# Kernel tuning notes

Measured on AMD Instinct MI355X. Metric: run time of the kernel, lower is better.

The kernel has to match this reference:

```python
import jax, jax.numpy as jnp
import numpy as np

A, B, K, P, STRIDE, ITERS = 32, 32, 3, 4, 2, 3
PSIZE = P * P
EPS = 1e-8


def add_patches(x):
    # x: (b, h, w, A*PSIZE) -> (b*oh*ow, K*K*A, PSIZE)
    b, h, w, c = x.shape
    oh = (h - K) // STRIDE + 1
    ow = (w - K) // STRIDE + 1
    idx = jnp.arange(oh) * STRIDE  # same for w since h == w here
    idx = idx[:, None] + jnp.arange(K)[None, :]          # (oh, K)
    p = x[:, idx]                                        # (b, oh, K, w, c)
    p = p[:, :, :, idx]                                  # (b, oh, K, ow, K, c)
    p = jnp.transpose(p, (0, 1, 3, 2, 4, 5))             # (b, oh, ow, K, K, c)
    p = p.reshape(b * oh * ow, K * K * A, PSIZE)
    return p, oh, ow


def transform_view(p_in, weights):
    # p_in: (N, K*K*A, PSIZE); weights: (K*K*A, B, P, P)
    N = p_in.shape[0]
    x = p_in.reshape(N, K * K * A, P, P)
    # pose matmul per (input capsule i, output type j): x[n,i] @ w[i,j]
    v = jnp.einsum('nipr,ijrq->nijpq', x, weights)       # (N, KKA, B, P, P)
    return v.reshape(N, K * K * A, B, PSIZE)


def squash(p):
    n2 = jnp.sum(p * p, axis=-1, keepdims=True)
    return p * n2 / (1.0 + n2) / jnp.sqrt(n2 + EPS)


def dynamic_routing(v, iters):
    # v: (N, KKA, B, PSIZE); inverted dynamic routing: softmax over input capsules
    N, KKA, Bt, _ = v.shape
    logits = jnp.zeros((N, KKA, Bt, 1), dtype=v.dtype)
    p = None
    for i in range(iters):
        r = jax.nn.softmax(logits, axis=1)               # route over input capsules
        p = squash(jnp.sum(r * v, axis=1, keepdims=True))  # (N,1,B,PSIZE)
        if i < iters - 1:
            logits = logits + jnp.sum(v * p, axis=-1, keepdims=True)
    return p[:, 0]                                       # (N, B, PSIZE)


def setup_inputs() -> dict:
    key = jax.random.key(0)
    k1, k2 = jax.random.split(key)
    x = jax.random.normal(k1, (2, 32, 32, A * PSIZE), dtype=jnp.float32)
    weights = jax.random.normal(k2, (K * K * A, B, P, P), dtype=jnp.float32)
    return {"x": x, "weights": weights}


def reference(x, weights):
    b = x.shape[0]
    p_in, oh, ow = add_patches(x)
    v = transform_view(p_in, weights)                    # (b*oh*ow, KKA, B, PSIZE)
    p_out = dynamic_routing(v, ITERS)                    # (b*oh*ow, B, PSIZE)
    return p_out.reshape(b, oh, ow, B * PSIZE)
```

## Files before the change

kernel.cpp:

```cpp
#include <hip/hip_runtime.h>


#define OH 15
#define OW 15
#define EPS_ 1e-8f

#define XT_ELEMS (2 * 32 * 32 * 512)
#define WT_ELEMS (32 * 5 * 64 * 16)

typedef float v2f __attribute__((ext_vector_type(2)));

__device__ __forceinline__ v2f pfma(float a, v2f b, v2f c) {
    return __builtin_elementwise_fma((v2f){a, a}, b, c);
}
__device__ __forceinline__ float b_lo(unsigned int u) {
    union { unsigned int i; float f; } c; c.i = u << 16; return c.f;
}
__device__ __forceinline__ float b_hi(unsigned int u) {
    union { unsigned int i; float f; } c; c.i = u & 0xFFFF0000u; return c.f;
}
__device__ __forceinline__ unsigned short f2bf(float f) {
    union { float f; unsigned int i; } c; c.f = f;
    return (unsigned short)((c.i + 0x7FFFu + ((c.i >> 16) & 1u)) >> 16);
}

__device__ __forceinline__ float dppx1(float x) {
    return __builtin_bit_cast(float, __builtin_amdgcn_update_dpp(
        0, __builtin_bit_cast(int, x), 0xB1, 0xF, 0xF, true));
}
__device__ __forceinline__ float dppx2(float x) {
    return __builtin_bit_cast(float, __builtin_amdgcn_update_dpp(
        0, __builtin_bit_cast(int, x), 0x4E, 0xF, 0xF, true));
}
template <int OFF>
__device__ __forceinline__ float swzx(float x) {
    return __builtin_bit_cast(float, __builtin_amdgcn_ds_swizzle(
        __builtin_bit_cast(int, x), OFF));
}
__device__ __forceinline__ float rdlane(float x, int q) {
    return __builtin_bit_cast(float, __builtin_amdgcn_readlane(
        __builtin_bit_cast(int, x), q));
}

__global__ __launch_bounds__(256) void stage_kernel(
    const float* __restrict__ x, const float* __restrict__ w,
    unsigned short* __restrict__ xt, unsigned short* __restrict__ wt)
{
    const int tid = blockIdx.x * 256 + threadIdx.x;
    if (tid < XT_ELEMS) {
        xt[tid] = f2bf(x[tid]);
    } else {
        const int t2 = tid - XT_ELEMS;
        const int j  = t2 / 5120;
        const int r  = t2 - j * 5120;
        const int k  = r >> 10;
        const int L  = (r >> 4) & 63;
        const int e  = r & 15;
        const int i  = L + 64 * k;
        wt[t2] = (i < 288) ? f2bf(w[(size_t)i * 512 + j * 16 + e])
                           : (unsigned short)0;
    }
}

template <bool PERM>
__global__ __launch_bounds__(64, 3) void convcaps_kernel(
    const void* __restrict__ xp,
    const void* __restrict__ wp_,
    float* __restrict__ out)
{
    const int blk  = blockIdx.x;
    const int n    = blk >> 5;
    const int j    = blk & 31;
    const int lane = threadIdx.x;

    const int batch = n / (OH * OW);
    const int rem   = n - batch * OH * OW;
    const int oy    = rem / OW;
    const int ox    = rem - oy * OW;

    const bool has5 = (lane < 32);

    v2f v[5][8];
    float logit[5] = {0.f, 0.f, 0.f, 0.f, has5 ? 0.f : -1e30f};

#pragma unroll
    for (int k = 0; k < 5; ++k) {
        if (k == 4 && !has5) {
#pragma unroll
            for (int m = 0; m < 8; ++m) v[4][m] = (v2f){0.f, 0.f};
        } else {
            const int i  = lane + 64 * k;
            const int a  = i & 31;
            const int kw = (i >> 5) % 3;
            const int kh = i / 96;
            const int h  = oy * 2 + kh;
            const int wc = ox * 2 + kw;
            const int pixel = (batch * 32 + h) * 32 + wc;

            float xr[16];
            v2f wr2[4][2];
            if (PERM) {
                const uint4* xb = reinterpret_cast<const uint4*>(
                    (const unsigned short*)xp + ((size_t)pixel * 512 + a * 16));
                uint4 u0 = xb[0], u1 = xb[1];
                xr[0]=b_lo(u0.x); xr[1]=b_hi(u0.x); xr[2]=b_lo(u0.y); xr[3]=b_hi(u0.y);
                xr[4]=b_lo(u0.z); xr[5]=b_hi(u0.z); xr[6]=b_lo(u0.w); xr[7]=b_hi(u0.w);
                xr[8]=b_lo(u1.x); xr[9]=b_hi(u1.x); xr[10]=b_lo(u1.y); xr[11]=b_hi(u1.y);
                xr[12]=b_lo(u1.z); xr[13]=b_hi(u1.z); xr[14]=b_lo(u1.w); xr[15]=b_hi(u1.w);
                const uint4* wb = reinterpret_cast<const uint4*>(
                    (const unsigned short*)wp_ + (((size_t)j * 5 + k) * 64 + lane) * 16);
                uint4 q0 = wb[0], q1 = wb[1];
                wr2[0][0] = (v2f){b_lo(q0.x), b_hi(q0.x)};
                wr2[0][1] = (v2f){b_lo(q0.y), b_hi(q0.y)};
                wr2[1][0] = (v2f){b_lo(q0.z), b_hi(q0.z)};
                wr2[1][1] = (v2f){b_lo(q0.w), b_hi(q0.w)};
                wr2[2][0] = (v2f){b_lo(q1.x), b_hi(q1.x)};
                wr2[2][1] = (v2f){b_lo(q1.y), b_hi(q1.y)};
                wr2[3][0] = (v2f){b_lo(q1.z), b_hi(q1.z)};
                wr2[3][1] = (v2f){b_lo(q1.w), b_hi(q1.w)};
            } else {
                const float4* xv = reinterpret_cast<const float4*>(
                    (const float*)xp + ((size_t)pixel * 512 + a * 16));
                float4 x0 = xv[0], x1 = xv[1], x2 = xv[2], x3 = xv[3];
                float t_[16] = { x0.x,x0.y,x0.z,x0.w, x1.x,x1.y,x1.z,x1.w,
                                 x2.x,x2.y,x2.z,x2.w, x3.x,x3.y,x3.z,x3.w };
#pragma unroll
                for (int e = 0; e < 16; ++e) xr[e] = t_[e];
                const float4* wq = reinterpret_cast<const float4*>(
                    (const float*)wp_ + ((size_t)i * 32 + j) * 16);
                float4 w0 = wq[0], w1 = wq[1], w2 = wq[2], w3 = wq[3];
                wr2[0][0]=(v2f){w0.x,w0.y}; wr2[0][1]=(v2f){w0.z,w0.w};
                wr2[1][0]=(v2f){w1.x,w1.y}; wr2[1][1]=(v2f){w1.z,w1.w};
                wr2[2][0]=(v2f){w2.x,w2.y}; wr2[2][1]=(v2f){w2.z,w2.w};
                wr2[3][0]=(v2f){w3.x,w3.y}; wr2[3][1]=(v2f){w3.z,w3.w};
            }

#pragma unroll
            for (int p = 0; p < 4; ++p) {
#pragma unroll
                for (int qq = 0; qq < 2; ++qq) {
                    v2f acc = (v2f){0.f, 0.f};
                    acc = pfma(xr[p*4+0], wr2[0][qq], acc);
                    acc = pfma(xr[p*4+1], wr2[1][qq], acc);
                    acc = pfma(xr[p*4+2], wr2[2][qq], acc);
                    acc = pfma(xr[p*4+3], wr2[3][qq], acc);
                    v[k][p*2+qq] = acc;
                }
            }
        }
    }

#pragma unroll
    for (int it = 0; it < 3; ++it) {
        v2f c2[8];
        float se_loc;
        if (it == 0) {
#pragma unroll
            for (int m = 0; m < 8; ++m)
                c2[m] = v[0][m] + v[1][m] + v[2][m] + v[3][m] + v[4][m];
            se_loc = 0.f;
        } else {
            const float e0 = __expf(logit[0]), e1 = __expf(logit[1]);
            const float e2 = __expf(logit[2]), e3 = __expf(logit[3]);
            const float e4 = __expf(logit[4]);
#pragma unroll
            for (int m = 0; m < 8; ++m)
                c2[m] = pfma(e0, v[0][m],
                        pfma(e1, v[1][m],
                        pfma(e2, v[2][m],
                        pfma(e3, v[3][m],
                        pfma(e4, v[4][m], (v2f){0.f, 0.f})))));
            se_loc = e0 + e1 + e2 + e3 + e4;
        }

        float c[16];
#pragma unroll
        for (int m = 0; m < 8; ++m) { c[2*m] = c2[m].x; c[2*m+1] = c2[m].y; }

        float seR = se_loc;
        float s8[8];
        {
            const bool b = lane & 1;
#pragma unroll
            for (int m = 0; m < 8; ++m) {
                float send = b ? c[2*m]   : c[2*m+1];
                float keep = b ? c[2*m+1] : c[2*m];
                s8[m] = keep + dppx1(send);
            }
            if (it > 0) seR += dppx1(seR);
        }
        float s4[4];
        {
            const bool b = (lane >> 1) & 1;
#pragma unroll
            for (int m = 0; m < 4; ++m) {
                float send = b ? s8[2*m]   : s8[2*m+1];
                float keep = b ? s8[2*m+1] : s8[2*m];
                s4[m] = keep + dppx2(send);
            }
            if (it > 0) seR += dppx2(seR);
        }
        float s2v[2];
        {
            const bool b = (lane >> 2) & 1;
#pragma unroll
            for (int m = 0; m < 2; ++m) {
                float send = b ? s4[2*m]   : s4[2*m+1];
                float keep = b ? s4[2*m+1] : s4[2*m];
                s2v[m] = keep + swzx<0x101F>(send);
            }
            if (it > 0) seR += swzx<0x101F>(seR);
        }
        float s1;
        {
            const bool b = (lane >> 3) & 1;
            float send = b ? s2v[0] : s2v[1];
            float keep = b ? s2v[1] : s2v[0];
            s1 = keep + swzx<0x201F>(send);
            if (it > 0) seR += swzx<0x201F>(seR);
        }
        s1 += swzx<0x401F>(s1);    if (it > 0) seR += swzx<0x401F>(seR);
        s1 += __shfl_xor(s1, 32);  if (it > 0) seR += __shfl_xor(seR, 32);

        const float s = (it == 0) ? s1 * (1.0f / 288.0f) : s1 / seR;

        float t2 = s * s;
        t2 += dppx1(t2);
        t2 += dppx2(t2);
        t2 += swzx<0x101F>(t2);
        t2 += swzx<0x201F>(t2);
        const float n2 = t2;
        const float scale = n2 / ((1.0f + n2) * sqrtf(n2 + EPS_));
        const float pval = s * scale;

        if (it < 2) {
            float pq[16];
#pragma unroll
            for (int q = 0; q < 16; ++q) pq[q] = rdlane(pval, q);
#pragma unroll
            for (int k = 0; k < 5; ++k) {
                float ax = 0.f, ay = 0.f;
#pragma unroll
                for (int m = 0; m < 8; ++m) {
                    ax = fmaf(v[k][m].x, pq[2*m],     ax);
                    ay = fmaf(v[k][m].y, pq[2*m + 1], ay);
                }
                logit[k] += ax + ay;
            }
        } else {
            if (lane < 16)
                out[(size_t)n * 512 + j * 16 + lane] = pval;
        }
    }
}

extern "C" void kernel_launch(void* const* d_in, const int* in_sizes, int n_in,
                              void* d_out, int out_size, void* d_ws, size_t ws_size,
                              hipStream_t stream) {
    const float* x = (const float*)d_in[0];
    const float* w = (const float*)d_in[1];
    float* out = (float*)d_out;
    const int nblocks = 450 * 32;

    const size_t need = (size_t)(XT_ELEMS + WT_ELEMS) * sizeof(unsigned short);
    if (d_ws != nullptr && ws_size >= need) {
        unsigned short* xt = (unsigned short*)d_ws;
        unsigned short* wt = xt + XT_ELEMS;
        stage_kernel<<<(XT_ELEMS + WT_ELEMS) / 256, 256, 0, stream>>>(x, w, xt, wt);
        convcaps_kernel<true><<<nblocks, 64, 0, stream>>>(xt, wt, out);
    } else {
        convcaps_kernel<false><<<nblocks, 64, 0, stream>>>(x, w, out);
    }
}
```

Measured before the change: 85.08 us.

## Raise occupancy, stream x unpacking, use fast rcp/rsq and packed logit FMAs

Raises the launch-bounds occupancy hint from 3 to 4 waves and unpacks the bf16 x values inside the compute loop instead of materialising a 16-float array, which lowers register pressure. Division and sqrt in the softmax normalisation and squash are replaced by hardware reciprocal and rsqrt intrinsics. The logit update now uses packed v2f FMAs. The risks are register spills under the tighter bound and small precision changes from the approximate rcp and rsq.

```diff
diff --git a/kernel.cpp b/kernel.cpp
--- a/kernel.cpp
+++ b/kernel.cpp
@@ -63,7 +63,7 @@
 }
 
 template <bool PERM>
-__global__ __launch_bounds__(64, 3) void convcaps_kernel(
+__global__ __launch_bounds__(64, 4) void convcaps_kernel(
     const void* __restrict__ xp,
     const void* __restrict__ wp_,
     float* __restrict__ out)
@@ -97,16 +97,11 @@
             const int wc = ox * 2 + kw;
             const int pixel = (batch * 32 + h) * 32 + wc;
 
-            float xr[16];
             v2f wr2[4][2];
             if (PERM) {
                 const uint4* xb = reinterpret_cast<const uint4*>(
                     (const unsigned short*)xp + ((size_t)pixel * 512 + a * 16));
                 uint4 u0 = xb[0], u1 = xb[1];
-                xr[0]=b_lo(u0.x); xr[1]=b_hi(u0.x); xr[2]=b_lo(u0.y); xr[3]=b_hi(u0.y);
-                xr[4]=b_lo(u0.z); xr[5]=b_hi(u0.z); xr[6]=b_lo(u0.w); xr[7]=b_hi(u0.w);
-                xr[8]=b_lo(u1.x); xr[9]=b_hi(u1.x); xr[10]=b_lo(u1.y); xr[11]=b_hi(u1.y);
-                xr[12]=b_lo(u1.z); xr[13]=b_hi(u1.z); xr[14]=b_lo(u1.w); xr[15]=b_hi(u1.w);
                 const uint4* wb = reinterpret_cast<const uint4*>(
                     (const unsigned short*)wp_ + (((size_t)j * 5 + k) * 64 + lane) * 16);
                 uint4 q0 = wb[0], q1 = wb[1];
@@ -118,14 +113,26 @@
                 wr2[2][1] = (v2f){b_lo(q1.y), b_hi(q1.y)};
                 wr2[3][0] = (v2f){b_lo(q1.z), b_hi(q1.z)};
                 wr2[3][1] = (v2f){b_lo(q1.w), b_hi(q1.w)};
+                const unsigned int dwp[8] = {u0.x, u0.y, u0.z, u0.w,
+                                             u1.x, u1.y, u1.z, u1.w};
+#pragma unroll
+                for (int p = 0; p < 4; ++p) {
+                    const unsigned int da = dwp[2*p], db = dwp[2*p+1];
+                    const float x0 = b_lo(da), x1 = b_hi(da);
+                    const float x2 = b_lo(db), x3 = b_hi(db);
+#pragma unroll
+                    for (int qq = 0; qq < 2; ++qq) {
+                        v2f acc = (v2f){0.f, 0.f};
+                        acc = pfma(x0, wr2[0][qq], acc);
+                        acc = pfma(x1, wr2[1][qq], acc);
+                        acc = pfma(x2, wr2[2][qq], acc);
+                        acc = pfma(x3, wr2[3][qq], acc);
+                        v[k][p*2+qq] = acc;
+                    }
+                }
             } else {
                 const float4* xv = reinterpret_cast<const float4*>(
                     (const float*)xp + ((size_t)pixel * 512 + a * 16));
-                float4 x0 = xv[0], x1 = xv[1], x2 = xv[2], x3 = xv[3];
-                float t_[16] = { x0.x,x0.y,x0.z,x0.w, x1.x,x1.y,x1.z,x1.w,
-                                 x2.x,x2.y,x2.z,x2.w, x3.x,x3.y,x3.z,x3.w };
-#pragma unroll
-                for (int e = 0; e < 16; ++e) xr[e] = t_[e];
                 const float4* wq = reinterpret_cast<const float4*>(
                     (const float*)wp_ + ((size_t)i * 32 + j) * 16);
                 float4 w0 = wq[0], w1 = wq[1], w2 = wq[2], w3 = wq[3];
@@ -133,18 +140,18 @@
                 wr2[1][0]=(v2f){w1.x,w1.y}; wr2[1][1]=(v2f){w1.z,w1.w};
                 wr2[2][0]=(v2f){w2.x,w2.y}; wr2[2][1]=(v2f){w2.z,w2.w};
                 wr2[3][0]=(v2f){w3.x,w3.y}; wr2[3][1]=(v2f){w3.z,w3.w};
-            }
-
-#pragma unroll
-            for (int p = 0; p < 4; ++p) {
-#pragma unroll
-                for (int qq = 0; qq < 2; ++qq) {
-                    v2f acc = (v2f){0.f, 0.f};
-                    acc = pfma(xr[p*4+0], wr2[0][qq], acc);
-                    acc = pfma(xr[p*4+1], wr2[1][qq], acc);
-                    acc = pfma(xr[p*4+2], wr2[2][qq], acc);
-                    acc = pfma(xr[p*4+3], wr2[3][qq], acc);
-                    v[k][p*2+qq] = acc;
+#pragma unroll
+                for (int p = 0; p < 4; ++p) {
+                    float4 xr4 = xv[p];
+#pragma unroll
+                    for (int qq = 0; qq < 2; ++qq) {
+                        v2f acc = (v2f){0.f, 0.f};
+                        acc = pfma(xr4.x, wr2[0][qq], acc);
+                        acc = pfma(xr4.y, wr2[1][qq], acc);
+                        acc = pfma(xr4.z, wr2[2][qq], acc);
+                        acc = pfma(xr4.w, wr2[3][qq], acc);
+                        v[k][p*2+qq] = acc;
+                    }
                 }
             }
         }
@@ -222,7 +229,8 @@
         s1 += swzx<0x401F>(s1);    if (it > 0) seR += swzx<0x401F>(seR);
         s1 += __shfl_xor(s1, 32);  if (it > 0) seR += __shfl_xor(seR, 32);
 
-        const float s = (it == 0) ? s1 * (1.0f / 288.0f) : s1 / seR;
+        const float s = (it == 0) ? s1 * (1.0f / 288.0f)
+                                  : s1 * __builtin_amdgcn_rcpf(seR);
 
         float t2 = s * s;
         t2 += dppx1(t2);
@@ -230,22 +238,22 @@
         t2 += swzx<0x101F>(t2);
         t2 += swzx<0x201F>(t2);
         const float n2 = t2;
-        const float scale = n2 / ((1.0f + n2) * sqrtf(n2 + EPS_));
+        const float scale = n2 * __builtin_amdgcn_rcpf(1.0f + n2)
+                               * __builtin_amdgcn_rsqf(n2 + EPS_);
         const float pval = s * scale;
 
         if (it < 2) {
-            float pq[16];
-#pragma unroll
-            for (int q = 0; q < 16; ++q) pq[q] = rdlane(pval, q);
+            v2f pq2[8];
+#pragma unroll
+            for (int m = 0; m < 8; ++m)
+                pq2[m] = (v2f){rdlane(pval, 2*m), rdlane(pval, 2*m+1)};
 #pragma unroll
             for (int k = 0; k < 5; ++k) {
-                float ax = 0.f, ay = 0.f;
-#pragma unroll
-                for (int m = 0; m < 8; ++m) {
-                    ax = fmaf(v[k][m].x, pq[2*m],     ax);
-                    ay = fmaf(v[k][m].y, pq[2*m + 1], ay);
-                }
-                logit[k] += ax + ay;
+                v2f acc = (v2f){0.f, 0.f};
+#pragma unroll
+                for (int m = 0; m < 8; ++m)
+                    acc = __builtin_elementwise_fma(v[k][m], pq2[m], acc);
+                logit[k] += acc.x + acc.y;
             }
         } else {
             if (lane < 16)
```

New measurement: 84.35 us. No clear change (-0.9%).
